# Kernel tuning notes

Measured on AMD Instinct MI355X. Metric: run time of the kernel, lower is better.

The kernel has to match this reference:

```python
import jax, jax.numpy as jnp
import numpy as np

N_NODES = 64
NUM_STEPS = 15
N_DP = 5
SLOPE = 25.0  # fast_sigmoid surrogate slope


def _spike(x):
    # forward Heaviside; surrogate grad only matters in bwd module
    return (x > 0).astype(x.dtype)


def _lif(x, mem, beta, thr):
    # snnTorch Leaky, reset_mechanism='subtract': reset from previous mem (detached)
    reset = jax.lax.stop_gradient((mem > thr).astype(x.dtype))
    mem = beta * mem + x - reset * thr
    spk = _spike(mem - thr)
    return spk, mem


def setup_inputs() -> dict:
    key = jax.random.key(0)
    ks = jax.random.split(key, 16)
    B = 2048
    def xavier(k, shape):
        fan_in, fan_out = shape
        lim = float(np.sqrt(6.0 / (fan_in + fan_out)))
        return jax.random.uniform(k, shape, jnp.float32, -lim, lim)
    return {
        "L_norm": jax.random.normal(ks[0], (B, N_NODES, N_NODES), jnp.float32),
        "X_seq": jax.random.normal(ks[1], (B, NUM_STEPS, N_NODES, 1), jnp.float32),
        "W_proj": xavier(ks[2], (1, 16)),   "b_proj": jnp.zeros((16,), jnp.float32),
        "W_gcn1": xavier(ks[3], (16, 32)),  "b_gcn1": jnp.zeros((32,), jnp.float32),
        "W_skip1": xavier(ks[4], (16, 32)), "b_skip1": jnp.zeros((32,), jnp.float32),
        "W_gcn2": xavier(ks[5], (32, 64)),  "b_gcn2": jnp.zeros((64,), jnp.float32),
        "W_skip2": xavier(ks[6], (32, 64)), "b_skip2": jnp.zeros((64,), jnp.float32),
        "W_c1": xavier(ks[7], (N_NODES * 64, 128)), "b_c1": jnp.zeros((128,), jnp.float32),
        "W_c2": xavier(ks[8], (128, 4)),    "b_c2": jnp.zeros((4,), jnp.float32),
    }


def reference(L_norm, X_seq, W_proj, b_proj, W_gcn1, b_gcn1, W_skip1, b_skip1,
              W_gcn2, b_gcn2, W_skip2, b_skip2, W_c1, b_c1, W_c2, b_c2):
    B = X_seq.shape[0]

    def hr_gcn(x, mems, Wg, bg, Ws, bs, betas, thrs):
        # dense Laplacian conv: (L @ (x W)) + b, plus triple LIF + linear skip
        cur = jnp.einsum("bnm,bmf->bnf", L_norm, x @ Wg) + bg
        spk_a, m_a = _lif(cur, mems[0], betas[0], thrs[0])
        spk_n, m_n = _lif(cur, mems[1], betas[1], thrs[1])
        spk_m, m_m = _lif(cur, mems[2], betas[2], thrs[2])
        spk_out = spk_a + spk_n + spk_m + (x @ Ws + bs)
        return spk_out, (m_a, m_n, m_m)

    z = lambda f: jnp.zeros((B, N_NODES, f), jnp.float32)
    carry0 = ((z(32),) * 3, (z(64),) * 3, z(64))

    def step(carry, x_t):
        mems1, mems2, mem_li = carry
        x = x_t @ W_proj + b_proj                      # [B, N, 16]
        spk1, mems1 = hr_gcn(x, mems1, W_gcn1, b_gcn1, W_skip1, b_skip1,
                             (0.8, 0.9, 0.95), (0.8, 1.0, 1.5))
        spk2, mems2 = hr_gcn(spk1, mems2, W_gcn2, b_gcn2, W_skip2, b_skip2,
                             (0.8, 0.9, 0.95), (0.8, 1.0, 1.5))
        mem_li = 0.9 * mem_li + spk2                   # Leaky, reset 'none'
        pot = mem_li.reshape(B, -1)                    # [B, N*64]
        return (mems1, mems2, mem_li), pot

    xs = jnp.swapaxes(X_seq, 0, 1)                     # [T, B, N, 1]
    _, pots = jax.lax.scan(step, carry0, xs)
    potentials = jnp.swapaxes(pots, 0, 1)              # [B, T, N*64]

    # DP decoder (dropout = identity in eval)
    dp_feat = potentials[:, -N_DP:, :].mean(axis=1) - potentials[:, :N_DP, :].mean(axis=1)
    h = jax.nn.relu(dp_feat @ W_c1 + b_c1)
    return h @ W_c2 + b_c2
```

## Files before the change

kernel.cpp:

```cpp
#include <hip/hip_runtime.h>
#include <hip/hip_bf16.h>


typedef __attribute__((ext_vector_type(8))) short s16x8;
typedef __attribute__((ext_vector_type(4))) float f32x4;
#define MFMA16(a, b, c) __builtin_amdgcn_mfma_f32_16x16x32_bf16(a, b, c, 0, 0, 0)

__device__ __forceinline__ short f2bs(float x) {
  union { __hip_bfloat16 h; short s; } u; u.h = __float2bfloat16(x); return u.s;
}
__device__ __forceinline__ float bs2f(short s) {
  union { short s; __hip_bfloat16 h; } u; u.s = s; return __bfloat162float(u.h);
}

#define LIF_STEP(mem, beta, thr, cur, spksum)                \
  {                                                          \
    float r_ = ((mem) > (thr)) ? (thr) : 0.0f;               \
    (mem) = (beta) * (mem) + (cur) - r_;                     \
    (spksum) += (((mem) - (thr)) > 0.0f) ? 1.0f : 0.0f;      \
  }

#define LFS 68
#define RS  36

__global__ __launch_bounds__(512, 2)
void hrsnn_main(const float* __restrict__ Lg,  const float* __restrict__ Xg,
                const float* __restrict__ Wp,  const float* __restrict__ bp,
                const float* __restrict__ Wg1, const float* __restrict__ bg1,
                const float* __restrict__ Ws1, const float* __restrict__ bs1,
                const float* __restrict__ Wg2, const float* __restrict__ bg2,
                const float* __restrict__ Ws2, const float* __restrict__ bs2,
                unsigned int* __restrict__ dp_out)
{
  __shared__ __align__(16) float UBUF[4608];
  float* const Lf    = UBUF;
  float* const S1row = UBUF;
  float* const Mrow  = UBUF + 2304;
  __shared__ __align__(16) short WgF[4 * 3 * 64 * 8];
  __shared__ __align__(16) unsigned int XtHL[960];
  __shared__ __align__(16) float Xtf[960];
  __shared__ float LxS[64], LsumS[64];
  __shared__ float u1A[32], cb1A[32], us1v[32], cs1v[32];
  __shared__ float u2gA[64], c2gA[64], u2sA[64], cs2A[64];

  const int tid = threadIdx.x;
  const int b = blockIdx.x;
  const int l = tid & 63, w = tid >> 6;
  const int p = w >> 1, h = w & 1;
  const int q = l >> 4, c = l & 15;
  const int R = 16 * p;

  const float* Lb = Lg + (size_t)b * 4096;
#pragma unroll
  for (int k = 0; k < 2; k++) {
    const int i4 = tid + 512 * k;
    const float4 v = *(const float4*)&Lb[i4 * 4];
    *(float4*)&Lf[(i4 >> 4) * LFS + (i4 & 15) * 4] = v;
  }
  const float* Xb = Xg + (size_t)b * 960;
  for (int i = tid; i < 960; i += 512) {
    const float x = Xb[i];
    const short hs = f2bs(x);
    const short ls = f2bs(x - bs2f(hs));
    XtHL[i] = ((unsigned int)(unsigned short)hs << 16) | (unsigned short)ls;
    Xtf[i] = x;
  }
  if (tid < 32) {
    const int f = tid;
    float a = 0.f, bb = 0.f, cc = 0.f, d = 0.f;
    for (int k = 0; k < 16; k++) {
      const float wp = Wp[k], bpv = bp[k];
      const float wg = Wg1[k * 32 + f], ws = Ws1[k * 32 + f];
      a += wp * wg; bb += bpv * wg;
      cc += wp * ws; d += bpv * ws;
    }
    u1A[f] = a; cb1A[f] = bb;
    us1v[f] = cc; cs1v[f] = d + bs1[f];
  }
  __syncthreads();

  {
    const int n = tid >> 3, o = tid & 7;
    const float4 a4 = *(const float4*)&Lf[n * LFS + 8 * o];
    const float4 b4 = *(const float4*)&Lf[n * LFS + 8 * o + 4];
    float ps = a4.x + a4.y + a4.z + a4.w + b4.x + b4.y + b4.z + b4.w;
    ps += __shfl_xor(ps, 1, 64);
    ps += __shfl_xor(ps, 2, 64);
    ps += __shfl_xor(ps, 4, 64);
    if (o == 0) LsumS[n] = ps;
  }
  s16x8 Lh[2], Lm[2], Ll[2];
#pragma unroll
  for (int s = 0; s < 2; s++) {
    const float* rp = &Lf[(R + c) * LFS + 32 * s + 8 * q];
    const float4 v0 = *(const float4*)rp;
    const float4 v1 = *(const float4*)(rp + 4);
    float v[8] = {v0.x, v0.y, v0.z, v0.w, v1.x, v1.y, v1.z, v1.w};
#pragma unroll
    for (int j = 0; j < 8; j++) {
      const short hh = f2bs(v[j]);       const float r1 = v[j] - bs2f(hh);
      const short mm = f2bs(r1);         const float r2 = r1 - bs2f(mm);
      Lh[s][j] = hh; Lm[s][j] = mm; Ll[s][j] = f2bs(r2);
    }
  }
  {
    const int tt = w & 3;
    float v[8];
#pragma unroll
    for (int j = 0; j < 8; j++) v[j] = Wg2[(8 * q + j) * 64 + 16 * tt + c];
    if (w < 4) {
      s16x8 fh, fm;
#pragma unroll
      for (int j = 0; j < 8; j++) {
        const short hh = f2bs(v[j]);
        fh[j] = hh; fm[j] = f2bs(v[j] - bs2f(hh));
      }
      *(s16x8*)&WgF[((tt * 3 + 0) * 64 + l) * 8] = fh;
      *(s16x8*)&WgF[((tt * 3 + 1) * 64 + l) * 8] = fm;
    } else {
      s16x8 fl;
#pragma unroll
      for (int j = 0; j < 8; j++) {
        const short hh = f2bs(v[j]);     const float r1 = v[j] - bs2f(hh);
        const short mm = f2bs(r1);       const float r2 = r1 - bs2f(mm);
        fl[j] = f2bs(r2);
      }
      *(s16x8*)&WgF[((tt * 3 + 2) * 64 + l) * 8] = fl;
    }
  }
  s16x8 WsH[2], WsL[2];
#pragma unroll
  for (int i = 0; i < 2; i++) {
    const int g0 = 32 * h + 16 * i;
#pragma unroll
    for (int j = 0; j < 8; j++) {
      const float x = Ws2[(8 * q + j) * 64 + g0 + c];
      const short hh = f2bs(x);
      WsH[i][j] = hh; WsL[i][j] = f2bs(x - bs2f(hh));
    }
  }
  __syncthreads();

  if (tid < 64) {
    const int g = tid;
    float a = 0.f, bb = 0.f, cc = 0.f, d = 0.f;
    for (int f = 0; f < 32; f++) {
      const float wg = Wg2[f * 64 + g], ws = Ws2[f * 64 + g];
      a += us1v[f] * wg; bb += cs1v[f] * wg;
      cc += us1v[f] * ws; d += cs1v[f] * ws;
    }
    u2gA[g] = a; c2gA[g] = bb; u2sA[g] = cc; cs2A[g] = d + bs2[g];
  }
  __syncthreads();

  float u2g2[2], u2s2[2], cs22[2], c2c[2][4];
#pragma unroll
  for (int i = 0; i < 2; i++) {
    const int g = 32 * h + 16 * i + c;
    u2g2[i] = u2gA[g]; u2s2[i] = u2sA[g]; cs22[i] = cs2A[g];
    const float cg = c2gA[g], bg = bg2[g];
#pragma unroll
    for (int r = 0; r < 4; r++) c2c[i][r] = LsumS[R + 4 * q + r] * cg + bg;
  }
  const int f1 = tid & 31, nb = tid >> 5;
  const float u1f = u1A[f1];
  float k1c[4];
  {
    const float cb = cb1A[f1], bg = bg1[f1];
#pragma unroll
    for (int j = 0; j < 4; j++) k1c[j] = LsumS[nb + 16 * j] * cb + bg;
  }

  float m1a[4], m1n[4], m1m[4];
#pragma unroll
  for (int j = 0; j < 4; j++) { m1a[j] = 0.f; m1n[j] = 0.f; m1m[j] = 0.f; }
  float m2a[2][4], m2n[2][4], m2m[2][4], mli[2][4], dpa[2][4];
#pragma unroll
  for (int i = 0; i < 2; i++)
#pragma unroll
    for (int r = 0; r < 4; r++) {
      m2a[i][r] = 0.f; m2n[i][r] = 0.f; m2m[i][r] = 0.f;
      mli[i][r] = 0.f; dpa[i][r] = 0.f;
    }

  const f32x4 fz = {0.f, 0.f, 0.f, 0.f};
  __syncthreads();

  for (int t = 0; t < 15; t++) {
    f32x4 lx = fz;
#pragma unroll
    for (int s = 0; s < 2; s++) {
      const unsigned int* xw = &XtHL[t * 64 + 32 * s + 8 * q];
      const uint4 w0 = *(const uint4*)xw;
      const uint4 w1 = *(const uint4*)(xw + 4);
      unsigned int wv[8] = {w0.x, w0.y, w0.z, w0.w, w1.x, w1.y, w1.z, w1.w};
      s16x8 bh, bl;
#pragma unroll
      for (int j = 0; j < 8; j++) {
        bh[j] = (short)(wv[j] >> 16);
        bl[j] = (short)(wv[j] & 0xffff);
      }
      lx = MFMA16(Lh[s], bh, lx);
      lx = MFMA16(Lm[s], bh, lx);
      lx = MFMA16(Lh[s], bl, lx);
    }
    if (h == 0 && c == 0) {
#pragma unroll
      for (int r = 0; r < 4; r++) LxS[R + 4 * q + r] = lx[r];
    }
    __syncthreads();

#pragma unroll
    for (int j = 0; j < 4; j++) {
      const int n = nb + 16 * j;
      const float cur = LxS[n] * u1f + k1c[j];
      float ss = 0.f;
      LIF_STEP(m1a[j], 0.8f, 0.8f, cur, ss);
      LIF_STEP(m1n[j], 0.9f, 1.0f, cur, ss);
      LIF_STEP(m1m[j], 0.95f, 1.5f, cur, ss);
      S1row[n * RS + f1] = ss;
    }
    __syncthreads();

    f32x4 macc = fz;
#pragma unroll
    for (int s = 0; s < 2; s++) {
      s16x8 bS;
#pragma unroll
      for (int j = 0; j < 8; j++)
        bS[j] = f2bs(S1row[(32 * s + 8 * q + j) * RS + 16 * h + c]);
      macc = MFMA16(Lh[s], bS, macc);
      macc = MFMA16(Lm[s], bS, macc);
      macc = MFMA16(Ll[s], bS, macc);
    }
#pragma unroll
    for (int r = 0; r < 4; r++) Mrow[(R + 4 * q + r) * RS + 16 * h + c] = macc[r];

    f32x4 sacc[2];
    {
      const float* rp = &S1row[(R + c) * RS + 8 * q];
      const float4 v0 = *(const float4*)rp;
      const float4 v1 = *(const float4*)(rp + 4);
      const float v[8] = {v0.x, v0.y, v0.z, v0.w, v1.x, v1.y, v1.z, v1.w};
      s16x8 aS;
#pragma unroll
      for (int j = 0; j < 8; j++) aS[j] = f2bs(v[j]);
#pragma unroll
      for (int i = 0; i < 2; i++) {
        sacc[i] = MFMA16(aS, WsH[i], fz);
        sacc[i] = MFMA16(aS, WsL[i], sacc[i]);
      }
    }
    __syncthreads();

    s16x8 aMh, aMm, aMl;
    {
      const float* rp = &Mrow[(R + c) * RS + 8 * q];
      const float4 v0 = *(const float4*)rp;
      const float4 v1 = *(const float4*)(rp + 4);
      const float v[8] = {v0.x, v0.y, v0.z, v0.w, v1.x, v1.y, v1.z, v1.w};
#pragma unroll
      for (int j = 0; j < 8; j++) {
        const short hh = f2bs(v[j]);     const float r1 = v[j] - bs2f(hh);
        const short mm = f2bs(r1);       const float r2 = r1 - bs2f(mm);
        aMh[j] = hh; aMm[j] = mm; aMl[j] = f2bs(r2);
      }
    }
    float xtn[4];
#pragma unroll
    for (int r = 0; r < 4; r++) xtn[r] = Xtf[t * 64 + R + 4 * q + r];

#pragma unroll
    for (int i = 0; i < 2; i++) {
      const int tt = 2 * h + i;
      const s16x8 bGh = *(const s16x8*)&WgF[((tt * 3 + 0) * 64 + l) * 8];
      const s16x8 bGm = *(const s16x8*)&WgF[((tt * 3 + 1) * 64 + l) * 8];
      const s16x8 bGl = *(const s16x8*)&WgF[((tt * 3 + 2) * 64 + l) * 8];
      f32x4 cacc = fz;
      cacc = MFMA16(aMh, bGh, cacc);
      cacc = MFMA16(aMh, bGm, cacc);
      cacc = MFMA16(aMm, bGh, cacc);
      cacc = MFMA16(aMh, bGl, cacc);
      cacc = MFMA16(aMm, bGm, cacc);
      cacc = MFMA16(aMl, bGh, cacc);
#pragma unroll
      for (int r = 0; r < 4; r++) {
        const float cur2 = cacc[r] + lx[r] * u2g2[i] + c2c[i][r];
        float ss = 0.f;
        LIF_STEP(m2a[i][r], 0.8f, 0.8f, cur2, ss);
        LIF_STEP(m2n[i][r], 0.9f, 1.0f, cur2, ss);
        LIF_STEP(m2m[i][r], 0.95f, 1.5f, cur2, ss);
        const float spk2 = ss + sacc[i][r] + xtn[r] * u2s2[i] + cs22[i];
        mli[i][r] = 0.9f * mli[i][r] + spk2;
      }
    }
    if (t < 5) {
#pragma unroll
      for (int i = 0; i < 2; i++)
#pragma unroll
        for (int r = 0; r < 4; r++) dpa[i][r] -= mli[i][r];
    } else if (t >= 10) {
#pragma unroll
      for (int i = 0; i < 2; i++)
#pragma unroll
        for (int r = 0; r < 4; r++) dpa[i][r] += mli[i][r];
    }
  }

  unsigned int* dpb = dp_out + (size_t)b * 4096;
#pragma unroll
  for (int i = 0; i < 2; i++) {
    const int g = 32 * h + 16 * i + c;
#pragma unroll
    for (int r = 0; r < 4; r++) {
      const int n = R + 4 * q + r;
      const float v = dpa[i][r] * 0.2f;
      const short hh = f2bs(v);
      const short ll = f2bs(v - bs2f(hh));
      dpb[n * 64 + g] = ((unsigned int)(unsigned short)hh << 16) | (unsigned short)ll;
    }
  }
}

__global__ __launch_bounds__(512, 1)
void hrsnn_decoder(const unsigned int* __restrict__ dpq, const float* __restrict__ W1,
                   const float* __restrict__ b1, const float* __restrict__ W2,
                   const float* __restrict__ b2, float* __restrict__ out)
{
  __shared__ __align__(16) float H[16][132];
  const int tid = threadIdx.x;
  const int l = tid & 63, tt = tid >> 6;
  const int q = l >> 4, c = l & 15;

  const unsigned int* arow = dpq + (size_t)(blockIdx.x * 16 + c) * 4096 + 8 * q;
  const float* bcol = W1 + (8 * q) * 128 + 16 * tt + c;

  f32x4 acc = {0.f, 0.f, 0.f, 0.f};
  for (int s = 0; s < 128; s++) {
    const uint4 a0 = *(const uint4*)(arow + 32 * s);
    const uint4 a1 = *(const uint4*)(arow + 32 * s + 4);
    const unsigned int av[8] = {a0.x, a0.y, a0.z, a0.w, a1.x, a1.y, a1.z, a1.w};
    s16x8 Ah, Al, Bh, Bl;
#pragma unroll
    for (int j = 0; j < 8; j++) {
      Ah[j] = (short)(av[j] >> 16);
      Al[j] = (short)(av[j] & 0xffff);
      const float x = bcol[(32 * s + j) * 128];
      const short hh = f2bs(x);
      Bh[j] = hh; Bl[j] = f2bs(x - bs2f(hh));
    }
    acc = MFMA16(Ah, Bh, acc);
    acc = MFMA16(Al, Bh, acc);
    acc = MFMA16(Ah, Bl, acc);
  }

  const float bk = b1[16 * tt + c];
#pragma unroll
  for (int r = 0; r < 4; r++) {
    const float hv = acc[r] + bk;
    H[4 * q + r][16 * tt + c] = hv > 0.f ? hv : 0.f;
  }
  __syncthreads();

  if (tid < 64) {
    const int i = tid >> 2, o = tid & 3;
    float s = b2[o];
    for (int k = 0; k < 128; k++) s += H[i][k] * W2[k * 4 + o];
    out[(size_t)(blockIdx.x * 16 + i) * 4 + o] = s;
  }
}

extern "C" void kernel_launch(void* const* d_in, const int* in_sizes, int n_in,
                              void* d_out, int out_size, void* d_ws, size_t ws_size,
                              hipStream_t stream)
{
  const float* Lg  = (const float*)d_in[0];
  const float* Xg  = (const float*)d_in[1];
  const float* Wp  = (const float*)d_in[2];
  const float* bp  = (const float*)d_in[3];
  const float* Wg1 = (const float*)d_in[4];
  const float* bg1 = (const float*)d_in[5];
  const float* Ws1 = (const float*)d_in[6];
  const float* bs1 = (const float*)d_in[7];
  const float* Wg2 = (const float*)d_in[8];
  const float* bg2 = (const float*)d_in[9];
  const float* Ws2 = (const float*)d_in[10];
  const float* bs2 = (const float*)d_in[11];
  const float* W1  = (const float*)d_in[12];
  const float* b1  = (const float*)d_in[13];
  const float* W2  = (const float*)d_in[14];
  const float* b2  = (const float*)d_in[15];

  unsigned int* dpq = (unsigned int*)d_ws;
  float* out = (float*)d_out;

  hipLaunchKernelGGL(hrsnn_main, dim3(2048), dim3(512), 0, stream,
                     Lg, Xg, Wp, bp, Wg1, bg1, Ws1, bs1, Wg2, bg2, Ws2, bs2, dpq);
  hipLaunchKernelGGL(hrsnn_decoder, dim3(128), dim3(512), 0, stream,
                     dpq, W1, b1, W2, b2, out);
}
```

Baseline: 472.4 us.

## Split decoder across column halves with LDS-staged W1 and transposed spike buffer

The decoder now launches 256 blocks of 256 threads. Each block handles 16 batch rows and half of the 128 hidden columns, stages W1 chunks into LDS pre-split into bf16 hi/lo, and uses two independent accumulators. Partial outputs are combined with atomicAdd after a memset of the output. The main kernel also writes a transposed copy of the layer-1 spikes so the MFMA B operand reads contiguous LDS, and its launch bounds are raised to 4 blocks per CU. The aims are more decoder parallelism, less redundant global W1 loading and conversion, and fewer LDS bank conflicts, at the cost of extra LDS, an extra memset launch, atomics, and register pressure from the higher occupancy target.

Measured after the change: 842.8 us. 78.4% more time.

```diff
diff --git a/kernel.cpp b/kernel.cpp
--- a/kernel.cpp
+++ b/kernel.cpp
@@ -22,8 +22,9 @@
 
 #define LFS 68
 #define RS  36
-
-__global__ __launch_bounds__(512, 2)
+#define TS  65
+
+__global__ __launch_bounds__(512, 4)
 void hrsnn_main(const float* __restrict__ Lg,  const float* __restrict__ Xg,
                 const float* __restrict__ Wp,  const float* __restrict__ bp,
                 const float* __restrict__ Wg1, const float* __restrict__ bg1,
@@ -36,6 +37,7 @@
   float* const Lf    = UBUF;
   float* const S1row = UBUF;
   float* const Mrow  = UBUF + 2304;
+  __shared__ __align__(16) float S1T[32 * TS];
   __shared__ __align__(16) short WgF[4 * 3 * 64 * 8];
   __shared__ __align__(16) unsigned int XtHL[960];
   __shared__ __align__(16) float Xtf[960];
@@ -219,6 +221,7 @@
       LIF_STEP(m1n[j], 0.9f, 1.0f, cur, ss);
       LIF_STEP(m1m[j], 0.95f, 1.5f, cur, ss);
       S1row[n * RS + f1] = ss;
+      S1T[f1 * TS + n] = ss;
     }
     __syncthreads();
 
@@ -228,7 +231,7 @@
       s16x8 bS;
 #pragma unroll
       for (int j = 0; j < 8; j++)
-        bS[j] = f2bs(S1row[(32 * s + 8 * q + j) * RS + 16 * h + c]);
+        bS[j] = f2bs(S1T[(16 * h + c) * TS + 32 * s + 8 * q + j]);
       macc = MFMA16(Lh[s], bS, macc);
       macc = MFMA16(Lm[s], bS, macc);
       macc = MFMA16(Ll[s], bS, macc);
@@ -322,51 +325,82 @@
   }
 }
 
-__global__ __launch_bounds__(512, 1)
-void hrsnn_decoder(const unsigned int* __restrict__ dpq, const float* __restrict__ W1,
+__global__ __launch_bounds__(256, 4)
+void hrsnn_decoder(const unsigned int* __restrict__ dpq,
+                   const float* __restrict__ W1,
                    const float* __restrict__ b1, const float* __restrict__ W2,
                    const float* __restrict__ b2, float* __restrict__ out)
 {
-  __shared__ __align__(16) float H[16][132];
+  __shared__ __align__(16) unsigned int T[128][65];
+  __shared__ __align__(16) float Hl[16][68];
   const int tid = threadIdx.x;
   const int l = tid & 63, tt = tid >> 6;
   const int q = l >> 4, c = l & 15;
-
-  const unsigned int* arow = dpq + (size_t)(blockIdx.x * 16 + c) * 4096 + 8 * q;
-  const float* bcol = W1 + (8 * q) * 128 + 16 * tt + c;
-
-  f32x4 acc = {0.f, 0.f, 0.f, 0.f};
-  for (int s = 0; s < 128; s++) {
-    const uint4 a0 = *(const uint4*)(arow + 32 * s);
-    const uint4 a1 = *(const uint4*)(arow + 32 * s + 4);
-    const unsigned int av[8] = {a0.x, a0.y, a0.z, a0.w, a1.x, a1.y, a1.z, a1.w};
-    s16x8 Ah, Al, Bh, Bl;
-#pragma unroll
-    for (int j = 0; j < 8; j++) {
-      Ah[j] = (short)(av[j] >> 16);
-      Al[j] = (short)(av[j] & 0xffff);
-      const float x = bcol[(32 * s + j) * 128];
-      const short hh = f2bs(x);
-      Bh[j] = hh; Bl[j] = f2bs(x - bs2f(hh));
-    }
-    acc = MFMA16(Ah, Bh, acc);
-    acc = MFMA16(Al, Bh, acc);
-    acc = MFMA16(Ah, Bl, acc);
-  }
-
-  const float bk = b1[16 * tt + c];
+  const int bt = blockIdx.x >> 1, ch = blockIdx.x & 1;
+  const int colg = ch * 64 + tt * 16 + c;
+
+  const unsigned int* ar = dpq + (size_t)(bt * 16 + c) * 4096 + 8 * q;
+  const float* wbase = W1 + ch * 64;
+
+  const f32x4 fz = {0.f, 0.f, 0.f, 0.f};
+  f32x4 acc0 = fz, acc1 = fz;
+  for (int kc = 0; kc < 32; kc++) {
+    __syncthreads();
+#pragma unroll
+    for (int u = 0; u < 8; u++) {
+      const int i4 = tid + 256 * u;
+      const int kk = i4 >> 4, c4 = (i4 & 15) * 4;
+      const float4 v = *(const float4*)&wbase[(size_t)(kc * 128 + kk) * 128 + c4];
+      const float vv[4] = {v.x, v.y, v.z, v.w};
+#pragma unroll
+      for (int e = 0; e < 4; e++) {
+        const short hh = f2bs(vv[e]);
+        const short ll = f2bs(vv[e] - bs2f(hh));
+        T[kk][c4 + e] = ((unsigned int)(unsigned short)hh << 16) | (unsigned short)ll;
+      }
+    }
+    __syncthreads();
+#pragma unroll
+    for (int sl = 0; sl < 4; sl++) {
+      const int s = 4 * kc + sl;
+      const uint4 a0 = *(const uint4*)(ar + 32 * s);
+      const uint4 a1 = *(const uint4*)(ar + 32 * s + 4);
+      const unsigned int av[8] = {a0.x, a0.y, a0.z, a0.w, a1.x, a1.y, a1.z, a1.w};
+      s16x8 Ah, Al, Bh, Bl;
+#pragma unroll
+      for (int j = 0; j < 8; j++) {
+        Ah[j] = (short)(av[j] >> 16);
+        Al[j] = (short)(av[j] & 0xffff);
+        const unsigned int bw = T[32 * sl + 8 * q + j][16 * tt + c];
+        Bh[j] = (short)(bw >> 16);
+        Bl[j] = (short)(bw & 0xffff);
+      }
+      if (sl & 1) {
+        acc1 = MFMA16(Ah, Bh, acc1);
+        acc1 = MFMA16(Al, Bh, acc1);
+        acc1 = MFMA16(Ah, Bl, acc1);
+      } else {
+        acc0 = MFMA16(Ah, Bh, acc0);
+        acc0 = MFMA16(Al, Bh, acc0);
+        acc0 = MFMA16(Ah, Bl, acc0);
+      }
+    }
+  }
+
+  const float bk = b1[colg];
 #pragma unroll
   for (int r = 0; r < 4; r++) {
-    const float hv = acc[r] + bk;
-    H[4 * q + r][16 * tt + c] = hv > 0.f ? hv : 0.f;
+    const float hv = acc0[r] + acc1[r] + bk;
+    Hl[4 * q + r][tt * 16 + c] = hv > 0.f ? hv : 0.f;
   }
   __syncthreads();
 
   if (tid < 64) {
     const int i = tid >> 2, o = tid & 3;
-    float s = b2[o];
-    for (int k = 0; k < 128; k++) s += H[i][k] * W2[k * 4 + o];
-    out[(size_t)(blockIdx.x * 16 + i) * 4 + o] = s;
+    float s = (ch == 0) ? b2[o] : 0.f;
+    for (int cc = 0; cc < 64; cc++)
+      s += Hl[i][cc] * W2[(ch * 64 + cc) * 4 + o];
+    atomicAdd(&out[(size_t)(bt * 16 + i) * 4 + o], s);
   }
 }
 
@@ -396,6 +430,7 @@
 
   hipLaunchKernelGGL(hrsnn_main, dim3(2048), dim3(512), 0, stream,
                      Lg, Xg, Wp, bp, Wg1, bg1, Ws1, bs1, Wg2, bg2, Ws2, bs2, dpq);
-  hipLaunchKernelGGL(hrsnn_decoder, dim3(128), dim3(512), 0, stream,
+  hipMemsetAsync(d_out, 0, (size_t)out_size * sizeof(float), stream);
+  hipLaunchKernelGGL(hrsnn_decoder, dim3(256), dim3(256), 0, stream,
                      dpq, W1, b1, W2, b2, out);
 }
```
